# Optimization experiments

Measured on AMD Instinct MI355X. Metric: run time of the kernel, lower is better.

## Reference

```python
import jax, jax.numpy as jnp
import numpy as np

B, S, D_IN, D_HID, D_OUT, H = 2, 2048, 1024, 1024, 1024, 16
HD = D_HID // H  # head_dim = 64


def setup_inputs() -> dict:
    key = jax.random.key(0)
    ks = jax.random.split(key, 9)
    s_in = 1.0 / np.sqrt(D_IN)
    s_out = 1.0 / np.sqrt(D_OUT)
    return {
        "x": jax.random.normal(ks[0], (B, S, D_IN), dtype=jnp.float32),
        "Wq": jax.random.uniform(ks[1], (D_IN, D_HID), jnp.float32, -s_in, s_in),
        "bq": jax.random.uniform(ks[2], (D_HID,), jnp.float32, -s_in, s_in),
        "Wk": jax.random.uniform(ks[3], (D_IN, D_HID), jnp.float32, -s_in, s_in),
        "bk": jax.random.uniform(ks[4], (D_HID,), jnp.float32, -s_in, s_in),
        "Wv": jax.random.uniform(ks[5], (D_IN, D_OUT), jnp.float32, -s_in, s_in),
        "bv": jax.random.uniform(ks[6], (D_OUT,), jnp.float32, -s_in, s_in),
        "Wo": jax.random.uniform(ks[7], (D_OUT, D_OUT), jnp.float32, -s_out, s_out),
        "bo": jax.random.uniform(ks[8], (D_OUT,), jnp.float32, -s_out, s_out),
    }


def reference(x, Wq, bq, Wk, bk, Wv, bv, Wo, bo):
    b, s, _ = x.shape
    q = (x @ Wq + bq).reshape(b, s, H, HD)  # [B,S,H,HD]
    k = (x @ Wk + bk).reshape(b, s, H, HD)
    v = (x @ Wv + bv).reshape(b, s, H, HD)
    scores = jnp.einsum("bqhd,bkhd->bhqk", q, k) / jnp.sqrt(jnp.float32(HD))
    attn = jax.nn.softmax(scores, axis=-1)  # [B,H,S,S]
    ctx = jnp.einsum("bhqk,bkhd->bqhd", attn, v).reshape(b, s, D_HID)
    return ctx @ Wo + bo
```

## Files before the change

kernel.cpp:

```cpp
#include <hip/hip_runtime.h>
#include <stdint.h>

typedef __attribute__((ext_vector_type(8))) short short8v;
typedef __attribute__((ext_vector_type(4))) float float4v;
typedef __attribute__((ext_vector_type(4))) unsigned short ushort4v;
typedef __attribute__((ext_vector_type(4))) float floatvec4;
typedef __attribute__((ext_vector_type(2))) unsigned int uint2v;

#define DEVI __device__ __forceinline__

DEVI unsigned short f2bf(float f) {
    unsigned int u = __builtin_bit_cast(unsigned int, f);
    u += 0x7FFFu + ((u >> 16) & 1u);
    return (unsigned short)(u >> 16);
}

DEVI unsigned int pk2bf(float a, float b) {
#if defined(__has_builtin) && __has_builtin(__builtin_amdgcn_cvt_pk_bf16_f32)
    auto r = __builtin_amdgcn_cvt_pk_bf16_f32(a, b);
    unsigned int u;
    __builtin_memcpy(&u, &r, 4);
    return u;
#else
    return (unsigned int)f2bf(a) | ((unsigned int)f2bf(b) << 16);
#endif
}

DEVI float ex2(float x) {
#if defined(__has_builtin) && __has_builtin(__builtin_amdgcn_exp2f)
    return __builtin_amdgcn_exp2f(x);
#else
    return __builtin_exp2f(x);
#endif
}

typedef __attribute__((address_space(1))) void GV;
typedef __attribute__((address_space(3))) void LV;
DEVI void gl2lds16(const void* g, void* l) {
    __builtin_amdgcn_global_load_lds((GV*)g, (LV*)l, 16, 0, 0);
}

__global__ void conv_x_kernel(const float* __restrict__ x, unsigned short* __restrict__ xb) {
    const int i = (blockIdx.x * 256 + threadIdx.x) * 4;
    const floatvec4 v = *(const floatvec4*)&x[i];
    ushort4v o;
#pragma unroll
    for (int r = 0; r < 4; r++) o[r] = f2bf(v[r]);
    *(ushort4v*)&xb[i] = o;
}

__global__ void transpose_w(const float* __restrict__ W, unsigned short* __restrict__ Wt) {
    __shared__ float t[32][33];
    const int tx = threadIdx.x, ty = threadIdx.y;
    const int bx = blockIdx.x, by = blockIdx.y;
#pragma unroll
    for (int i = 0; i < 4; i++)
        t[ty + i * 8][tx] = W[(size_t)(by * 32 + ty + i * 8) * 1024 + bx * 32 + tx];
    __syncthreads();
#pragma unroll
    for (int i = 0; i < 4; i++)
        Wt[(size_t)(bx * 32 + ty + i * 8) * 1024 + by * 32 + tx] = f2bf(t[tx][ty + i * 8]);
}

__global__ __launch_bounds__(256, 2) void qkv_gemm(
    const unsigned short* __restrict__ X, const unsigned short* __restrict__ Wt,
    const float* __restrict__ bq, const float* __restrict__ bk, const float* __restrict__ bv,
    unsigned short* __restrict__ qb, unsigned short* __restrict__ kb,
    unsigned short* __restrict__ vtb)
{
    __shared__ __align__(16) unsigned short As[128 * 32];
    __shared__ __align__(16) unsigned short Bs[128 * 32];
    const int tid = threadIdx.x, lane = tid & 63, wv = tid >> 6;
    const int quad = lane >> 4, l16 = lane & 15;
    const int w = blockIdx.x >> 3;
    const int n0 = (blockIdx.x & 7) * 128;
    const int row0 = blockIdx.y * 128;
    const unsigned short* Wsel = Wt + (size_t)w * (1024 * 1024);

    const int srow = lane >> 2;
    const int sg = (lane & 3) ^ ((lane >> 2) & 3) ^ ((lane >> 4) & 3);
    const int scol = sg * 8;
    const int fsw = (l16 & 3) ^ ((l16 >> 2) & 3);
    const int wm = (wv >> 1) * 64, wn = (wv & 1) * 64;

    float4v acc[4][4];
#pragma unroll
    for (int i = 0; i < 4; i++)
#pragma unroll
        for (int j = 0; j < 4; j++) acc[i][j] = (float4v){0.f, 0.f, 0.f, 0.f};

    for (int k0 = 0; k0 < 1024; k0 += 32) {
        __syncthreads();
#pragma unroll
        for (int i = 0; i < 2; i++) {
            const int c = wv * 2 + i;
            gl2lds16(X + (size_t)(row0 + c * 16 + srow) * 1024 + k0 + scol, As + c * 512);
            gl2lds16(Wsel + (size_t)(n0 + c * 16 + srow) * 1024 + k0 + scol, Bs + c * 512);
        }
        __syncthreads();
        short8v a[4], b[4];
#pragma unroll
        for (int mt = 0; mt < 4; mt++)
            a[mt] = *(const short8v*)&As[(wm + mt * 16 + l16) * 32 + ((quad ^ fsw) * 8)];
#pragma unroll
        for (int nt = 0; nt < 4; nt++)
            b[nt] = *(const short8v*)&Bs[(wn + nt * 16 + l16) * 32 + ((quad ^ fsw) * 8)];
#pragma unroll
        for (int mt = 0; mt < 4; mt++)
#pragma unroll
            for (int nt = 0; nt < 4; nt++)
                acc[mt][nt] = __builtin_amdgcn_mfma_f32_16x16x32_bf16(a[mt], b[nt], acc[mt][nt], 0, 0, 0);
    }

    const float* bias = (w == 0) ? bq : (w == 1) ? bk : bv;
    const float scl = (w == 0) ? 0.18033688011112042f : 1.0f;
#pragma unroll
    for (int nt = 0; nt < 4; nt++) {
        const int col = n0 + wn + nt * 16 + l16;
        const float bb = bias[col];
        const int h = col >> 6, hd = col & 63;
#pragma unroll
        for (int mt = 0; mt < 4; mt++) {
            const int tok0 = row0 + wm + mt * 16 + quad * 4;
            const int b_ = tok0 >> 11, s0 = tok0 & 2047;
            if (w == 2) {
                ushort4v pk;
#pragma unroll
                for (int r = 0; r < 4; r++) pk[r] = f2bf(acc[mt][nt][r] + bb);
                *(ushort4v*)&vtb[(((size_t)b_ * 16 + h) * 64 + hd) * 2048 + s0] = pk;
            } else {
                unsigned short* dst = (w == 0) ? qb : kb;
#pragma unroll
                for (int r = 0; r < 4; r++)
                    dst[(((size_t)b_ * 16 + h) * 2048 + (s0 + r)) * 64 + hd] =
                        f2bf((acc[mt][nt][r] + bb) * scl);
            }
        }
    }
}

__global__ __launch_bounds__(256, 2) void attn_kernel(
    const unsigned short* __restrict__ qb, const unsigned short* __restrict__ kb,
    const unsigned short* __restrict__ vtb, unsigned short* __restrict__ ctxb)
{
    __shared__ __align__(16) unsigned short Kt[128 * 64];
    __shared__ __align__(16) unsigned short Vt[64 * 128];
    __shared__ __align__(16) unsigned short Pb[4][32 * 128];
    const int tid = threadIdx.x, lane = tid & 63, wv = tid >> 6;
    const int quad = lane >> 4, l16 = lane & 15;
    const int bh = blockIdx.x, qt = blockIdx.y;
    const size_t boff = (size_t)bh * (2048 * 64);
    const unsigned short* qp = qb + boff;
    const unsigned short* kp = kb + boff;
    const unsigned short* vp = vtb + boff;
    const int q0 = qt * 128 + wv * 32;

    short8v qf[2][2];
#pragma unroll
    for (int nt = 0; nt < 2; nt++)
#pragma unroll
        for (int kc = 0; kc < 2; kc++)
            qf[nt][kc] = *(const short8v*)&qp[(size_t)(q0 + nt * 16 + l16) * 64 + kc * 32 + quad * 8];

    float4v accO[2][4];
#pragma unroll
    for (int nt = 0; nt < 2; nt++)
#pragma unroll
        for (int ht = 0; ht < 4; ht++) accO[nt][ht] = (float4v){0.f, 0.f, 0.f, 0.f};
    float lsum[2] = {0.f, 0.f};

    const int krow = lane >> 3;
    const int kg = (lane & 7) ^ (lane >> 3);
    const int vrow = lane >> 4;
    const int rsw = l16 & 7;

    const int ktb0 = l16 * 64 + ((quad ^ rsw) * 8);
    const int ktb1 = l16 * 64 + (((4 + quad) ^ rsw) * 8);
    const int pbase = l16 * 128 + (((quad >> 1) ^ (l16 & 1)) * 8) + ((quad & 1) * 4);
    const int le = (l16 & 14) * 8;
    const int prb = l16 * 128 + ((quad ^ (l16 & 3)) * 8);
    const int l12e = (l16 & 12) * 8;

    for (int kt0 = 0; kt0 < 2048; kt0 += 128) {
        __syncthreads();
#pragma unroll
        for (int i = 0; i < 4; i++) {
            const int c = wv * 4 + i;
            gl2lds16(kp + (size_t)(kt0 + c * 8 + krow) * 64 + kg * 8, Kt + c * 512);
            const int vr = c * 4 + vrow;
            const int vg = (lane & 15) ^ (vr & 15);
            gl2lds16(vp + (size_t)vr * 2048 + kt0 + vg * 8, Vt + c * 512);
        }
        __syncthreads();

#pragma unroll
        for (int mt = 0; mt < 8; mt++) {
            const short8v a0 = *(const short8v*)&Kt[ktb0 + mt * 1024];
            const short8v a1 = *(const short8v*)&Kt[ktb1 + mt * 1024];
            const int poff = pbase + ((mt * 16) ^ le);
#pragma unroll
            for (int nt = 0; nt < 2; nt++) {
                float4v z = (float4v){0.f, 0.f, 0.f, 0.f};
                z = __builtin_amdgcn_mfma_f32_16x16x32_bf16(a0, qf[nt][0], z, 0, 0, 0);
                z = __builtin_amdgcn_mfma_f32_16x16x32_bf16(a1, qf[nt][1], z, 0, 0, 0);
                const float p0 = ex2(z[0]), p1 = ex2(z[1]);
                const float p2 = ex2(z[2]), p3 = ex2(z[3]);
                lsum[nt] += (p0 + p1) + (p2 + p3);
                *(uint2v*)&Pb[wv][poff + nt * 2048] = (uint2v){pk2bf(p0, p1), pk2bf(p2, p3)};
            }
        }
        asm volatile("s_waitcnt lgkmcnt(0)" ::: "memory");

#pragma unroll
        for (int kc = 0; kc < 4; kc++) {
            const int roff = (kc * 32) ^ l12e;
            const short8v ap0 = *(const short8v*)&Pb[wv][prb + roff];
            const short8v ap1 = *(const short8v*)&Pb[wv][prb + roff + 2048];
#pragma unroll
            for (int ht = 0; ht < 4; ht++) {
                const short8v bv8 = *(const short8v*)&Vt[prb + roff + ht * 2048];
                accO[0][ht] = __builtin_amdgcn_mfma_f32_16x16x32_bf16(ap0, bv8, accO[0][ht], 0, 0, 0);
                accO[1][ht] = __builtin_amdgcn_mfma_f32_16x16x32_bf16(ap1, bv8, accO[1][ht], 0, 0, 0);
            }
        }
    }

#pragma unroll
    for (int nt = 0; nt < 2; nt++) {
        lsum[nt] += __shfl_xor(lsum[nt], 16);
        lsum[nt] += __shfl_xor(lsum[nt], 32);
    }

    const int b_ = bh >> 4, h = bh & 15;
#pragma unroll
    for (int nt = 0; nt < 2; nt++)
#pragma unroll
        for (int r = 0; r < 4; r++) {
            const int s = q0 + nt * 16 + quad * 4 + r;
            const float inv = 1.0f / __shfl(lsum[nt], quad * 4 + r);
#pragma unroll
            for (int ht = 0; ht < 4; ht++) {
                const int hd = ht * 16 + l16;
                ctxb[((size_t)(b_ * 2048 + s)) * 1024 + h * 64 + hd] = f2bf(accO[nt][ht][r] * inv);
            }
        }
}

__global__ __launch_bounds__(256, 2) void out_gemm(
    const unsigned short* __restrict__ ctx, const unsigned short* __restrict__ Wot,
    const float* __restrict__ bo, float* __restrict__ out)
{
    __shared__ __align__(16) unsigned short As[128 * 32];
    __shared__ __align__(16) unsigned short Bs[128 * 32];
    const int tid = threadIdx.x, lane = tid & 63, wv = tid >> 6;
    const int quad = lane >> 4, l16 = lane & 15;
    const int n0 = blockIdx.x * 128;
    const int row0 = blockIdx.y * 128;

    const int srow = lane >> 2;
    const int sg = (lane & 3) ^ ((lane >> 2) & 3) ^ ((lane >> 4) & 3);
    const int scol = sg * 8;
    const int fsw = (l16 & 3) ^ ((l16 >> 2) & 3);
    const int wm = (wv >> 1) * 64, wn = (wv & 1) * 64;

    float4v acc[4][4];
#pragma unroll
    for (int i = 0; i < 4; i++)
#pragma unroll
        for (int j = 0; j < 4; j++) acc[i][j] = (float4v){0.f, 0.f, 0.f, 0.f};

    for (int k0 = 0; k0 < 1024; k0 += 32) {
        __syncthreads();
#pragma unroll
        for (int i = 0; i < 2; i++) {
            const int c = wv * 2 + i;
            gl2lds16(ctx + (size_t)(row0 + c * 16 + srow) * 1024 + k0 + scol, As + c * 512);
            gl2lds16(Wot + (size_t)(n0 + c * 16 + srow) * 1024 + k0 + scol, Bs + c * 512);
        }
        __syncthreads();
        short8v a[4], b[4];
#pragma unroll
        for (int mt = 0; mt < 4; mt++)
            a[mt] = *(const short8v*)&As[(wm + mt * 16 + l16) * 32 + ((quad ^ fsw) * 8)];
#pragma unroll
        for (int nt = 0; nt < 4; nt++)
            b[nt] = *(const short8v*)&Bs[(wn + nt * 16 + l16) * 32 + ((quad ^ fsw) * 8)];
#pragma unroll
        for (int mt = 0; mt < 4; mt++)
#pragma unroll
            for (int nt = 0; nt < 4; nt++)
                acc[mt][nt] = __builtin_amdgcn_mfma_f32_16x16x32_bf16(a[mt], b[nt], acc[mt][nt], 0, 0, 0);
    }

#pragma unroll
    for (int nt = 0; nt < 4; nt++) {
        const int col = n0 + wn + nt * 16 + l16;
        const float bb = bo[col];
#pragma unroll
        for (int mt = 0; mt < 4; mt++) {
            const int tok0 = row0 + wm + mt * 16 + quad * 4;
#pragma unroll
            for (int r = 0; r < 4; r++)
                out[(size_t)(tok0 + r) * 1024 + col] = acc[mt][nt][r] + bb;
        }
    }
}

extern "C" void kernel_launch(void* const* d_in, const int* in_sizes, int n_in,
                              void* d_out, int out_size, void* d_ws, size_t ws_size,
                              hipStream_t stream) {
    const float* x  = (const float*)d_in[0];
    const float* Wq = (const float*)d_in[1];
    const float* bq = (const float*)d_in[2];
    const float* Wk = (const float*)d_in[3];
    const float* bk = (const float*)d_in[4];
    const float* Wv = (const float*)d_in[5];
    const float* bv = (const float*)d_in[6];
    const float* Wo = (const float*)d_in[7];
    const float* bo = (const float*)d_in[8];
    float* out = (float*)d_out;

    char* ws = (char*)d_ws;
    unsigned short* xb   = (unsigned short*)(ws);
    unsigned short* qbuf = (unsigned short*)(ws + (8u << 20));
    unsigned short* kbuf = (unsigned short*)(ws + (16u << 20));
    unsigned short* vtb  = (unsigned short*)(ws + (24u << 20));
    unsigned short* wt   = (unsigned short*)(ws + (32u << 20));
    unsigned short* wot  = (unsigned short*)(ws + (38u << 20));

    conv_x_kernel<<<4096, 256, 0, stream>>>(x, xb);
    dim3 tb(32, 8);
    transpose_w<<<dim3(32, 32), tb, 0, stream>>>(Wq, wt);
    transpose_w<<<dim3(32, 32), tb, 0, stream>>>(Wk, wt + (1u << 20));
    transpose_w<<<dim3(32, 32), tb, 0, stream>>>(Wv, wt + (2u << 20));
    transpose_w<<<dim3(32, 32), tb, 0, stream>>>(Wo, wot);

    qkv_gemm<<<dim3(24, 32), 256, 0, stream>>>(xb, wt, bq, bk, bv, qbuf, kbuf, vtb);
    attn_kernel<<<dim3(32, 16), 256, 0, stream>>>(qbuf, kbuf, vtb, xb );
    out_gemm<<<dim3(8, 32), 256, 0, stream>>>(xb, wot, bo, out);
}
```

Measured before the change: 214.5 us.

## Interleave QK and PV per 32-key chunk with small P buffer, merge weight transposes

The attention inner loop now processes keys in 32-wide chunks, computing scores, writing them to a small per-wave P buffer and immediately consuming them for the PV MFMAs. This replaces the full 128-wide P staging, cutting LDS from 64KB to about 40KB per block, and launch bounds are raised to 4 blocks per CU to increase occupancy. The four weight-transpose launches are merged into one launch with a z dimension to reduce launch overhead. The tradeoff is more waitcnt barriers per tile and possible register pressure under the tighter launch bound.

```diff
diff --git a/kernel.cpp b/kernel.cpp
--- a/kernel.cpp
+++ b/kernel.cpp
@@ -2,6 +2,7 @@
 #include <stdint.h>
 
 typedef __attribute__((ext_vector_type(8))) short short8v;
+typedef __attribute__((ext_vector_type(4))) short short4v;
 typedef __attribute__((ext_vector_type(4))) float float4v;
 typedef __attribute__((ext_vector_type(4))) unsigned short ushort4v;
 typedef __attribute__((ext_vector_type(4))) float floatvec4;
@@ -49,17 +50,22 @@
     *(ushort4v*)&xb[i] = o;
 }
 
-__global__ void transpose_w(const float* __restrict__ W, unsigned short* __restrict__ Wt) {
+__global__ void transpose_w4(const float* __restrict__ W0, const float* __restrict__ W1,
+                             const float* __restrict__ W2, const float* __restrict__ W3,
+                             unsigned short* __restrict__ D0, unsigned short* __restrict__ D1,
+                             unsigned short* __restrict__ D2, unsigned short* __restrict__ D3) {
     __shared__ float t[32][33];
     const int tx = threadIdx.x, ty = threadIdx.y;
-    const int bx = blockIdx.x, by = blockIdx.y;
+    const int bx = blockIdx.x, by = blockIdx.y, z = blockIdx.z;
+    const float* W = (z == 0) ? W0 : (z == 1) ? W1 : (z == 2) ? W2 : W3;
+    unsigned short* D = (z == 0) ? D0 : (z == 1) ? D1 : (z == 2) ? D2 : D3;
 #pragma unroll
     for (int i = 0; i < 4; i++)
         t[ty + i * 8][tx] = W[(size_t)(by * 32 + ty + i * 8) * 1024 + bx * 32 + tx];
     __syncthreads();
 #pragma unroll
     for (int i = 0; i < 4; i++)
-        Wt[(size_t)(bx * 32 + ty + i * 8) * 1024 + by * 32 + tx] = f2bf(t[tx][ty + i * 8]);
+        D[(size_t)(bx * 32 + ty + i * 8) * 1024 + by * 32 + tx] = f2bf(t[tx][ty + i * 8]);
 }
 
 __global__ __launch_bounds__(256, 2) void qkv_gemm(
@@ -139,13 +145,13 @@
     }
 }
 
-__global__ __launch_bounds__(256, 2) void attn_kernel(
+__global__ __launch_bounds__(256, 4) void attn_kernel(
     const unsigned short* __restrict__ qb, const unsigned short* __restrict__ kb,
     const unsigned short* __restrict__ vtb, unsigned short* __restrict__ ctxb)
 {
     __shared__ __align__(16) unsigned short Kt[128 * 64];
     __shared__ __align__(16) unsigned short Vt[64 * 128];
-    __shared__ __align__(16) unsigned short Pb[4][32 * 128];
+    __shared__ __align__(16) unsigned short Pbs[4][32 * 32];
     const int tid = threadIdx.x, lane = tid & 63, wv = tid >> 6;
     const int quad = lane >> 4, l16 = lane & 15;
     const int bh = blockIdx.x, qt = blockIdx.y;
@@ -176,10 +182,14 @@
 
     const int ktb0 = l16 * 64 + ((quad ^ rsw) * 8);
     const int ktb1 = l16 * 64 + (((4 + quad) ^ rsw) * 8);
-    const int pbase = l16 * 128 + (((quad >> 1) ^ (l16 & 1)) * 8) + ((quad & 1) * 4);
-    const int le = (l16 & 14) * 8;
-    const int prb = l16 * 128 + ((quad ^ (l16 & 3)) * 8);
+    const int vrb = l16 * 128 + ((quad ^ (l16 & 3)) * 8);
     const int l12e = (l16 & 12) * 8;
+    const int pwb = l16 * 32 + ((quad ^ ((l16 >> 1) & 3)) * 4);
+    const int hsw = (l16 >> 3) & 1;
+    const int s1 = (l16 >> 1) & 1;
+    const int prbase = l16 * 32 + ((quad ^ ((l16 >> 2) & 3)) * 8);
+    const int pr0 = prbase + s1 * 4;
+    const int pr1 = prbase + (1 - s1) * 4;
 
     for (int kt0 = 0; kt0 < 2048; kt0 += 128) {
         __syncthreads();
@@ -194,33 +204,39 @@
         __syncthreads();
 
 #pragma unroll
-        for (int mt = 0; mt < 8; mt++) {
-            const short8v a0 = *(const short8v*)&Kt[ktb0 + mt * 1024];
-            const short8v a1 = *(const short8v*)&Kt[ktb1 + mt * 1024];
-            const int poff = pbase + ((mt * 16) ^ le);
+        for (int kc = 0; kc < 4; kc++) {
+#pragma unroll
+            for (int h = 0; h < 2; h++) {
+                const int mt = kc * 2 + h;
+                const short8v a0 = *(const short8v*)&Kt[ktb0 + mt * 1024];
+                const short8v a1 = *(const short8v*)&Kt[ktb1 + mt * 1024];
+                const int hoff = (h ^ hsw) * 16;
+#pragma unroll
+                for (int nt = 0; nt < 2; nt++) {
+                    float4v z = (float4v){0.f, 0.f, 0.f, 0.f};
+                    z = __builtin_amdgcn_mfma_f32_16x16x32_bf16(a0, qf[nt][0], z, 0, 0, 0);
+                    z = __builtin_amdgcn_mfma_f32_16x16x32_bf16(a1, qf[nt][1], z, 0, 0, 0);
+                    const float p0 = ex2(z[0]), p1 = ex2(z[1]);
+                    const float p2 = ex2(z[2]), p3 = ex2(z[3]);
+                    lsum[nt] += (p0 + p1) + (p2 + p3);
+                    *(uint2v*)&Pbs[wv][pwb + hoff + nt * 512] =
+                        (uint2v){pk2bf(p0, p1), pk2bf(p2, p3)};
+                }
+            }
+            short8v bvv[4];
+            const int roff = (kc * 32) ^ l12e;
+#pragma unroll
+            for (int ht = 0; ht < 4; ht++)
+                bvv[ht] = *(const short8v*)&Vt[vrb + roff + ht * 2048];
+            asm volatile("s_waitcnt lgkmcnt(0)" ::: "memory");
 #pragma unroll
             for (int nt = 0; nt < 2; nt++) {
-                float4v z = (float4v){0.f, 0.f, 0.f, 0.f};
-                z = __builtin_amdgcn_mfma_f32_16x16x32_bf16(a0, qf[nt][0], z, 0, 0, 0);
-                z = __builtin_amdgcn_mfma_f32_16x16x32_bf16(a1, qf[nt][1], z, 0, 0, 0);
-                const float p0 = ex2(z[0]), p1 = ex2(z[1]);
-                const float p2 = ex2(z[2]), p3 = ex2(z[3]);
-                lsum[nt] += (p0 + p1) + (p2 + p3);
-                *(uint2v*)&Pb[wv][poff + nt * 2048] = (uint2v){pk2bf(p0, p1), pk2bf(p2, p3)};
-            }
-        }
-        asm volatile("s_waitcnt lgkmcnt(0)" ::: "memory");
-
-#pragma unroll
-        for (int kc = 0; kc < 4; kc++) {
-            const int roff = (kc * 32) ^ l12e;
-            const short8v ap0 = *(const short8v*)&Pb[wv][prb + roff];
-            const short8v ap1 = *(const short8v*)&Pb[wv][prb + roff + 2048];
-#pragma unroll
-            for (int ht = 0; ht < 4; ht++) {
-                const short8v bv8 = *(const short8v*)&Vt[prb + roff + ht * 2048];
-                accO[0][ht] = __builtin_amdgcn_mfma_f32_16x16x32_bf16(ap0, bv8, accO[0][ht], 0, 0, 0);
-                accO[1][ht] = __builtin_amdgcn_mfma_f32_16x16x32_bf16(ap1, bv8, accO[1][ht], 0, 0, 0);
+                const short4v d0 = *(const short4v*)&Pbs[wv][pr0 + nt * 512];
+                const short4v d1 = *(const short4v*)&Pbs[wv][pr1 + nt * 512];
+                const short8v ap = __builtin_shufflevector(d0, d1, 0, 1, 2, 3, 4, 5, 6, 7);
+#pragma unroll
+                for (int ht = 0; ht < 4; ht++)
+                    accO[nt][ht] = __builtin_amdgcn_mfma_f32_16x16x32_bf16(ap, bvv[ht], accO[nt][ht], 0, 0, 0);
             }
         }
     }
@@ -329,11 +345,8 @@
     unsigned short* wot  = (unsigned short*)(ws + (38u << 20));
 
     conv_x_kernel<<<4096, 256, 0, stream>>>(x, xb);
-    dim3 tb(32, 8);
-    transpose_w<<<dim3(32, 32), tb, 0, stream>>>(Wq, wt);
-    transpose_w<<<dim3(32, 32), tb, 0, stream>>>(Wk, wt + (1u << 20));
-    transpose_w<<<dim3(32, 32), tb, 0, stream>>>(Wv, wt + (2u << 20));
-    transpose_w<<<dim3(32, 32), tb, 0, stream>>>(Wo, wot);
+    transpose_w4<<<dim3(32, 32, 4), dim3(32, 8), 0, stream>>>(
+        Wq, Wk, Wv, Wo, wt, wt + (1u << 20), wt + (2u << 20), wot);
 
     qkv_gemm<<<dim3(24, 32), 256, 0, stream>>>(xb, wt, bq, bk, bv, qbuf, kbuf, vtb);
     attn_kernel<<<dim3(32, 16), 256, 0, stream>>>(qbuf, kbuf, vtb, xb );
```

After: 220.6 us. 2.8% more time.
